# Kernel tuning notes

Hardware: AMD Instinct MI355X
Metric: run time of the kernel (lower is better)

## Reference

```python
import jax, jax.numpy as jnp
import numpy as np

NEG_SLOPE = 0.2
EPS = 1e-9


def setup_inputs() -> dict:
    key = jax.random.key(0)
    ks = jax.random.split(key, 6)
    B, N, E, H, F = 2, 40000, 640000, 4, 32
    X = jax.random.normal(ks[0], (B, N, H, F), dtype=jnp.float32)
    A_self = jax.random.normal(ks[1], (H, F), dtype=jnp.float32)
    A_adjc = jax.random.normal(ks[2], (H, F), dtype=jnp.float32)
    targets = jax.random.randint(ks[3], (B, E), 0, N, dtype=jnp.int32)
    sources = jax.random.randint(ks[4], (B, E), 0, N, dtype=jnp.int32)
    degree = jax.random.uniform(ks[5], (B, E), dtype=jnp.float32)
    return {"X": X, "A_self": A_self, "A_adjc": A_adjc, "degree": degree,
            "targets": targets, "sources": sources, "N": N}


def reference(X, A_self, A_adjc, degree, targets, sources, N):
    # X: [B, N, H, F]; targets/sources: [B, E]
    # per-node attention logits: [B, N, H]
    e_self = jnp.einsum("bnhf,hf->bnh", X, A_self)
    e_adjc = jnp.einsum("bnhf,hf->bnh", X, A_adjc)
    # gather to edges: [B, E, H]
    es = jnp.take_along_axis(e_self, targets[:, :, None], axis=1)
    ea = jnp.take_along_axis(e_adjc, sources[:, :, None], axis=1)
    e = jax.nn.leaky_relu(es + ea, negative_slope=NEG_SLOPE)

    seg_max = jax.vmap(lambda v, i: jax.ops.segment_max(v, i, num_segments=N))
    seg_sum = jax.vmap(lambda v, i: jax.ops.segment_sum(v, i, num_segments=N))

    # exact normalization from source: exp(e - seg_max(e)), then divide by
    # seg_max of the exponentials (+eps), both gathered back to edges.
    m1 = jnp.take_along_axis(seg_max(e, targets), targets[:, :, None], axis=1)
    e = jnp.exp(e - m1)
    m2 = jnp.take_along_axis(seg_max(e, targets), targets[:, :, None], axis=1)
    attn = (e / (m2 + EPS))[..., None]  # [B, E, H, 1]; dropout omitted (eval)

    # message passing: gather source features, weight, scatter-sum to targets
    msg = jnp.take_along_axis(X, sources[:, :, None, None], axis=1) * attn  # [B,E,H,F]
    out = seg_sum(msg, targets)  # [B, N, H, F]
    return out
```

## Files before the change

### kernel.cpp

```cpp
#include <hip/hip_runtime.h>
#include <stdint.h>

#define BB     2
#define NNODE  40000
#define NEDGE  640000
#define NH     4
#define NF     32
#define NHF    128
#define SEGN   (BB * NNODE)
#define GEDGE  (BB * NEDGE)
#define SLOT   48

#define W      512
#define NBK_B  79
#define NBK    (BB * NBK_B)
#define CAP    9216
#define BLK_E  2048
#define NBLKA  (GEDGE / BLK_E)

static constexpr float NEG_SLOPE = 0.2f;
static constexpr float NEG_BIG   = -3.4e38f;

__global__ void prep_k(const float* __restrict__ X,
                       const float* __restrict__ As,
                       const float* __restrict__ Aa,
                       float* __restrict__ S, float* __restrict__ A,
                       unsigned* __restrict__ cursor) {
    int idx = blockIdx.x * blockDim.x + threadIdx.x;
    if (idx < NBK) cursor[idx] = 0u;
    if (idx >= SEGN * NH) return;
    int h = idx & (NH - 1);
    const float4* xv = (const float4*)(X + (size_t)idx * NF);
    const float4* sv = (const float4*)(As + h * NF);
    const float4* av = (const float4*)(Aa + h * NF);
    float s = 0.f, a = 0.f;
#pragma unroll
    for (int i = 0; i < 8; ++i) {
        float4 x = xv[i];
        float4 ws = sv[i];
        float4 wa = av[i];
        s += x.x * ws.x + x.y * ws.y + x.z * ws.z + x.w * ws.w;
        a += x.x * wa.x + x.y * wa.y + x.z * wa.z + x.w * wa.w;
    }
    S[idx] = s;
    A[idx] = a;
}

__global__ __launch_bounds__(256) void binA_k(const int* __restrict__ tg,
                                              const int* __restrict__ sc,
                                              unsigned* __restrict__ cursor,
                                              unsigned* __restrict__ pairs) {
    __shared__ unsigned hist[NBK];
    __shared__ unsigned lofs[NBK];
    __shared__ unsigned gofs[NBK];
    __shared__ unsigned wsum[4];
    __shared__ unsigned staged[BLK_E];
    __shared__ unsigned char sbk[BLK_E];
    int t = threadIdx.x;
    int base = blockIdx.x * BLK_E;
    for (int i = t; i < NBK; i += 256) hist[i] = 0u;
    __syncthreads();

    unsigned pr[8];
    unsigned short pbk[8], plp[8];
#pragma unroll
    for (int k = 0; k < 8; ++k) {
        int e = base + k * 256 + t;
        int tgv = tg[e], scv = sc[e];
        int b = (e >= NEDGE) ? 1 : 0;
        unsigned bk = (unsigned)(b * NBK_B + (tgv >> 9));
        pr[k]  = ((unsigned)(tgv & (W - 1)) << 16) | (unsigned)scv;
        pbk[k] = (unsigned short)bk;
        plp[k] = (unsigned short)atomicAdd(&hist[bk], 1u);
    }
    __syncthreads();
    {
        int lane = t & 63, w = t >> 6;
        unsigned v = (t < NBK) ? hist[t] : 0u;
        unsigned inc = v;
#pragma unroll
        for (int d = 1; d < 64; d <<= 1) {
            unsigned u = __shfl_up(inc, d);
            if (lane >= d) inc += u;
        }
        if (lane == 63) wsum[w] = inc;
        __syncthreads();
        unsigned woff = 0;
#pragma unroll
        for (int i = 0; i < 3; ++i) { if (i < w) woff += wsum[i]; }
        if (t < NBK) {
            lofs[t] = woff + inc - v;
            if (v > 0u)
                gofs[t] = atomicAdd(&cursor[t], v);
        }
    }
    __syncthreads();
#pragma unroll
    for (int k = 0; k < 8; ++k) {
        unsigned j = lofs[pbk[k]] + plp[k];
        staged[j] = pr[k];
        sbk[j] = (unsigned char)pbk[k];
    }
    __syncthreads();
    for (int j = t; j < BLK_E; j += 256) {
        unsigned bk = sbk[j];
        unsigned dst = gofs[bk] + ((unsigned)j - lofs[bk]);
        if (dst < CAP)
            pairs[(size_t)bk * CAP + dst] = staged[j];
    }
}

__global__ __launch_bounds__(1024) void binB_k(const unsigned* __restrict__ cursor,
                                               const unsigned* __restrict__ pairs,
                                               unsigned short* __restrict__ srt,
                                               unsigned* __restrict__ deg) {
    __shared__ unsigned short loc[W * SLOT];
    __shared__ unsigned dloc[W];
    int t = threadIdx.x;
    int gbk = blockIdx.x;
    int b = gbk / NBK_B;
    int bkloc = gbk - b * NBK_B;
    int node0 = b * NNODE + bkloc * W;
    int wEff = min(W, NNODE - bkloc * W);
    for (int i = t; i < W; i += 1024) dloc[i] = 0u;
    __syncthreads();
    int nE = (int)min(cursor[gbk], (unsigned)CAP);
    const unsigned* pb = pairs + (size_t)gbk * CAP;
    for (int j = t; j < nE; j += 1024) {
        unsigned p = pb[j];
        unsigned tl = p >> 16;
        unsigned pos = atomicAdd(&dloc[tl], 1u);
        if (pos < SLOT)
            loc[tl * SLOT + pos] = (unsigned short)(p & 0xFFFFu);
    }
    __syncthreads();
    unsigned* srt32 = (unsigned*)(srt + (size_t)node0 * SLOT);
    const unsigned* loc32 = (const unsigned*)loc;
    int n32 = wEff * SLOT / 2;
    for (int i = t; i < n32; i += 1024) srt32[i] = loc32[i];
    for (int i = t; i < wEff; i += 1024) deg[node0 + i] = dloc[i];
}

__global__ __launch_bounds__(256) void gather_k(
        const float* __restrict__ X, const float* __restrict__ S,
        const float* __restrict__ A, const unsigned* __restrict__ deg,
        const unsigned short* __restrict__ srt, float* __restrict__ OUT) {
    int node = blockIdx.x * 4 + (threadIdx.x >> 6);
    int t = threadIdx.x & 63;
    int hs = t & 3;
    int es = t >> 2;
    int h32 = t >> 5;
    int q = t & 31;
    int haq = q >> 3;
    int dg = min((int)deg[node], SLOT);
    int bbase = (node >= NNODE) ? NNODE : 0;
    size_t beg = (size_t)node * SLOT;

    float sh = S[node * NH + hs];

    float v[3];
    int   sb[3];
#pragma unroll
    for (int c = 0; c < 3; ++c) {
        int e = 16 * c + es;
        int s0 = bbase;
        float vv = NEG_BIG;
        if (e < dg) {
            s0 = bbase + (int)srt[beg + e];
            vv = sh + A[s0 * NH + hs];
            vv = vv > 0.f ? vv : NEG_SLOPE * vv;
        }
        sb[c] = s0;
        v[c]  = vv;
    }
    float m = fmaxf(fmaxf(v[0], v[1]), v[2]);
    m = fmaxf(m, __shfl_xor(m, 4));
    m = fmaxf(m, __shfl_xor(m, 8));
    m = fmaxf(m, __shfl_xor(m, 16));
    m = fmaxf(m, __shfl_xor(m, 32));
    float w[3];
#pragma unroll
    for (int c = 0; c < 3; ++c)
        w[c] = (16 * c + es < dg) ? __expf(v[c] - m) : 0.f;

    float4 acc = make_float4(0.f, 0.f, 0.f, 0.f);
#pragma unroll
    for (int i = 0; i < 24; ++i) {
        if (2 * i < dg) {
            int e2 = 2 * i + h32;
            float we  = __shfl(w[i >> 3],  4 * (e2 & 15) + haq);
            int   sbe = __shfl(sb[i >> 3], 4 * (e2 & 15));
            const float4 x = *(const float4*)(X + (size_t)sbe * NHF + 4 * q);
            acc.x += x.x * we;
            acc.y += x.y * we;
            acc.z += x.z * we;
            acc.w += x.w * we;
        }
    }
    acc.x += __shfl_xor(acc.x, 32);
    acc.y += __shfl_xor(acc.y, 32);
    acc.z += __shfl_xor(acc.z, 32);
    acc.w += __shfl_xor(acc.w, 32);
    if (t < 32) {
        float4* o = (float4*)(OUT + (size_t)node * NHF + 4 * q);
        *o = acc;
    }
}

extern "C" void kernel_launch(void* const* d_in, const int* in_sizes, int n_in,
                              void* d_out, int out_size, void* d_ws, size_t ws_size,
                              hipStream_t stream) {
    const float* X  = (const float*)d_in[0];
    const float* As = (const float*)d_in[1];
    const float* Aa = (const float*)d_in[2];
    const int* tg = (const int*)d_in[4];
    const int* sc = (const int*)d_in[5];
    float* OUT = (float*)d_out;

    char* ws = (char*)d_ws;
    float*          S      = (float*)ws;
    float*          A      = (float*)(ws + 1280000);
    unsigned*       deg    = (unsigned*)(ws + 2560000);
    unsigned*       cursor = (unsigned*)(ws + 2880000);
    unsigned*       pairs  = (unsigned*)(ws + 2880640);
    unsigned short* srt    = (unsigned short*)(ws + 8705152);

    const int nlog = SEGN * NH;
    prep_k<<<(nlog + 255) / 256, 256, 0, stream>>>(X, As, Aa, S, A, cursor);
    binA_k<<<NBLKA, 256, 0, stream>>>(tg, sc, cursor, pairs);
    binB_k<<<NBK, 1024, 0, stream>>>(cursor, pairs, srt, deg);
    gather_k<<<SEGN / 4, 256, 0, stream>>>(X, S, A, deg, srt, OUT);
}
```

Measured before the change: 219.2 us.

## Fuse four pipeline kernels into one cooperative persistent kernel with grid syncs

Merges the prep, two binning passes and the gather into a single persistent cooperative kernel. Stages are separated by grid-wide syncs instead of separate launches. The second binning pass is split into half-buckets of 256 nodes at 256 threads per block, and nontemporal loads and stores are used for the streaming edge and pair buffers. This removes per-launch gaps and tail effects. The costs are grid.sync overhead, lower occupancy limits, and each half-task reading its whole bucket's pairs twice.

```diff
diff --git a/kernel.cpp b/kernel.cpp
--- a/kernel.cpp
+++ b/kernel.cpp
@@ -1,5 +1,8 @@
 #include <hip/hip_runtime.h>
+#include <hip/hip_cooperative_groups.h>
 #include <stdint.h>
+
+namespace cg = cooperative_groups;
 
 #define BB     2
 #define NNODE  40000
@@ -16,16 +19,218 @@
 #define NBK    (BB * NBK_B)
 #define CAP    9216
 #define BLK_E  2048
-#define NBLKA  (GEDGE / BLK_E)
+#define NCHUNK (GEDGE / BLK_E)
+#define MAXG   1536
 
 static constexpr float NEG_SLOPE = 0.2f;
 static constexpr float NEG_BIG   = -3.4e38f;
 
-__global__ void prep_k(const float* __restrict__ X,
-                       const float* __restrict__ As,
-                       const float* __restrict__ Aa,
-                       float* __restrict__ S, float* __restrict__ A,
-                       unsigned* __restrict__ cursor) {
+union SharedU {
+    struct {
+        unsigned hist[NBK], lofs[NBK], gofs[NBK], wsum[4];
+        unsigned staged[BLK_E];
+        unsigned char sbk[BLK_E];
+    } a;
+    struct {
+        unsigned short loc[256 * SLOT];
+        unsigned dloc[256];
+    } b;
+};
+
+__global__ __launch_bounds__(256, 6) void mega_k(
+        const int* __restrict__ tg, const int* __restrict__ sc,
+        const float* __restrict__ X,
+        const float* __restrict__ As, const float* __restrict__ Aa,
+        float* __restrict__ S, float* __restrict__ A,
+        unsigned* __restrict__ cursor, unsigned* __restrict__ pairs,
+        unsigned short* __restrict__ srt, unsigned* __restrict__ deg,
+        float* __restrict__ OUT) {
+    __shared__ SharedU shm;
+    cg::grid_group grid = cg::this_grid();
+    int t = threadIdx.x;
+    int gtid = blockIdx.x * 256 + t;
+    int gsz = gridDim.x * 256;
+
+    for (int idx = gtid; idx < SEGN * NH; idx += gsz) {
+        int h = idx & (NH - 1);
+        const float4* xv = (const float4*)(X + (size_t)idx * NF);
+        const float4* sv = (const float4*)(As + h * NF);
+        const float4* av = (const float4*)(Aa + h * NF);
+        float s = 0.f, a = 0.f;
+#pragma unroll
+        for (int i = 0; i < 8; ++i) {
+            float4 x = xv[i];
+            float4 ws = sv[i];
+            float4 wa = av[i];
+            s += x.x * ws.x + x.y * ws.y + x.z * ws.z + x.w * ws.w;
+            a += x.x * wa.x + x.y * wa.y + x.z * wa.z + x.w * wa.w;
+        }
+        S[idx] = s;
+        A[idx] = a;
+    }
+    for (int i = gtid; i < NBK; i += gsz) cursor[i] = 0u;
+    grid.sync();
+
+    for (int chunk = blockIdx.x; chunk < NCHUNK; chunk += gridDim.x) {
+        int base = chunk * BLK_E;
+        for (int i = t; i < NBK; i += 256) shm.a.hist[i] = 0u;
+        __syncthreads();
+
+        unsigned pr[8];
+        unsigned short pbk[8], plp[8];
+#pragma unroll
+        for (int k = 0; k < 8; ++k) {
+            int e = base + k * 256 + t;
+            int tgv = __builtin_nontemporal_load(tg + e);
+            int scv = __builtin_nontemporal_load(sc + e);
+            int b = (e >= NEDGE) ? 1 : 0;
+            unsigned bk = (unsigned)(b * NBK_B + (tgv >> 9));
+            pr[k]  = ((unsigned)(tgv & (W - 1)) << 16) | (unsigned)scv;
+            pbk[k] = (unsigned short)bk;
+            plp[k] = (unsigned short)atomicAdd(&shm.a.hist[bk], 1u);
+        }
+        __syncthreads();
+        {
+            int lane = t & 63, w = t >> 6;
+            unsigned v = (t < NBK) ? shm.a.hist[t] : 0u;
+            unsigned inc = v;
+#pragma unroll
+            for (int d = 1; d < 64; d <<= 1) {
+                unsigned u = __shfl_up(inc, d);
+                if (lane >= d) inc += u;
+            }
+            if (lane == 63) shm.a.wsum[w] = inc;
+            __syncthreads();
+            unsigned woff = 0;
+#pragma unroll
+            for (int i = 0; i < 3; ++i) { if (i < w) woff += shm.a.wsum[i]; }
+            if (t < NBK) {
+                shm.a.lofs[t] = woff + inc - v;
+                if (v > 0u)
+                    shm.a.gofs[t] = atomicAdd(&cursor[t], v);
+            }
+        }
+        __syncthreads();
+#pragma unroll
+        for (int k = 0; k < 8; ++k) {
+            unsigned j = shm.a.lofs[pbk[k]] + plp[k];
+            shm.a.staged[j] = pr[k];
+            shm.a.sbk[j] = (unsigned char)pbk[k];
+        }
+        __syncthreads();
+        for (int j = t; j < BLK_E; j += 256) {
+            unsigned bk = shm.a.sbk[j];
+            unsigned dst = shm.a.gofs[bk] + ((unsigned)j - shm.a.lofs[bk]);
+            if (dst < CAP)
+                __builtin_nontemporal_store(shm.a.staged[j],
+                                            pairs + (size_t)bk * CAP + dst);
+        }
+        __syncthreads();
+    }
+    grid.sync();
+
+    for (int task = blockIdx.x; task < NBK * 2; task += gridDim.x) {
+        int gbk = task >> 1, half = task & 1;
+        int b = gbk / NBK_B;
+        int bkloc = gbk - b * NBK_B;
+        int nstart = bkloc * W + half * 256;
+        int wEff = min(256, NNODE - nstart);
+        shm.b.dloc[t] = 0u;
+        __syncthreads();
+        int nE = (wEff > 0) ? (int)min(cursor[gbk], (unsigned)CAP) : 0;
+        const unsigned* pb = pairs + (size_t)gbk * CAP;
+        for (int j = t; j < nE; j += 256) {
+            unsigned p = __builtin_nontemporal_load(pb + j);
+            int tl = (int)(p >> 16) - half * 256;
+            if (0 <= tl && tl < 256) {
+                unsigned pos = atomicAdd(&shm.b.dloc[tl], 1u);
+                if (pos < SLOT)
+                    shm.b.loc[tl * SLOT + pos] = (unsigned short)(p & 0xFFFFu);
+            }
+        }
+        __syncthreads();
+        if (wEff > 0) {
+            int node0 = b * NNODE + nstart;
+            unsigned* srt32 = (unsigned*)(srt + (size_t)node0 * SLOT);
+            const unsigned* loc32 = (const unsigned*)shm.b.loc;
+            int n32 = wEff * SLOT / 2;
+            for (int i = t; i < n32; i += 256)
+                __builtin_nontemporal_store(loc32[i], srt32 + i);
+            for (int i = t; i < wEff; i += 256)
+                __builtin_nontemporal_store(shm.b.dloc[i], deg + node0 + i);
+        }
+        __syncthreads();
+    }
+    grid.sync();
+
+    {
+        int lane = t & 63;
+        int wv = t >> 6;
+        int hs = lane & 3;
+        int es = lane >> 2;
+        int h32 = lane >> 5;
+        int q = lane & 31;
+        int haq = q >> 3;
+        for (int node = blockIdx.x * 4 + wv; node < SEGN; node += gridDim.x * 4) {
+            int dg = min((int)deg[node], SLOT);
+            int bbase = (node >= NNODE) ? NNODE : 0;
+            size_t beg = (size_t)node * SLOT;
+            float sH = S[node * NH + hs];
+
+            float v[3];
+            int   sb[3];
+#pragma unroll
+            for (int c = 0; c < 3; ++c) {
+                int e = 16 * c + es;
+                int s0 = bbase;
+                float vv = NEG_BIG;
+                if (e < dg) {
+                    s0 = bbase + (int)srt[beg + e];
+                    vv = sH + A[s0 * NH + hs];
+                    vv = vv > 0.f ? vv : NEG_SLOPE * vv;
+                }
+                sb[c] = s0;
+                v[c]  = vv;
+            }
+            float m = fmaxf(fmaxf(v[0], v[1]), v[2]);
+            m = fmaxf(m, __shfl_xor(m, 4));
+            m = fmaxf(m, __shfl_xor(m, 8));
+            m = fmaxf(m, __shfl_xor(m, 16));
+            m = fmaxf(m, __shfl_xor(m, 32));
+            float w[3];
+#pragma unroll
+            for (int c = 0; c < 3; ++c)
+                w[c] = (16 * c + es < dg) ? __expf(v[c] - m) : 0.f;
+
+            float4 acc = make_float4(0.f, 0.f, 0.f, 0.f);
+#pragma unroll
+            for (int i = 0; i < 24; ++i) {
+                if (2 * i < dg) {
+                    int e2 = 2 * i + h32;
+                    float we  = __shfl(w[i >> 3],  4 * (e2 & 15) + haq);
+                    int   sbe = __shfl(sb[i >> 3], 4 * (e2 & 15));
+                    const float4 x = *(const float4*)(X + (size_t)sbe * NHF + 4 * q);
+                    acc.x += x.x * we;
+                    acc.y += x.y * we;
+                    acc.z += x.z * we;
+                    acc.w += x.w * we;
+                }
+            }
+            acc.x += __shfl_xor(acc.x, 32);
+            acc.y += __shfl_xor(acc.y, 32);
+            acc.z += __shfl_xor(acc.z, 32);
+            acc.w += __shfl_xor(acc.w, 32);
+            if (lane < 32) {
+                float4* o = (float4*)(OUT + (size_t)node * NHF + 4 * q);
+                *o = acc;
+            }
+        }
+    }
+}
+
+__global__ void prep_k(const float* __restrict__ X, const float* __restrict__ As,
+                       const float* __restrict__ Aa, float* __restrict__ S,
+                       float* __restrict__ A, unsigned* __restrict__ cursor) {
     int idx = blockIdx.x * blockDim.x + threadIdx.x;
     if (idx < NBK) cursor[idx] = 0u;
     if (idx >= SEGN * NH) return;
@@ -36,9 +241,7 @@
     float s = 0.f, a = 0.f;
 #pragma unroll
     for (int i = 0; i < 8; ++i) {
-        float4 x = xv[i];
-        float4 ws = sv[i];
-        float4 wa = av[i];
+        float4 x = xv[i], ws = sv[i], wa = av[i];
         s += x.x * ws.x + x.y * ws.y + x.z * ws.z + x.w * ws.w;
         a += x.x * wa.x + x.y * wa.y + x.z * wa.z + x.w * wa.w;
     }
@@ -50,17 +253,13 @@
                                               const int* __restrict__ sc,
                                               unsigned* __restrict__ cursor,
                                               unsigned* __restrict__ pairs) {
-    __shared__ unsigned hist[NBK];
-    __shared__ unsigned lofs[NBK];
-    __shared__ unsigned gofs[NBK];
-    __shared__ unsigned wsum[4];
+    __shared__ unsigned hist[NBK], lofs[NBK], gofs[NBK], wsum[4];
     __shared__ unsigned staged[BLK_E];
     __shared__ unsigned char sbk[BLK_E];
     int t = threadIdx.x;
     int base = blockIdx.x * BLK_E;
     for (int i = t; i < NBK; i += 256) hist[i] = 0u;
     __syncthreads();
-
     unsigned pr[8];
     unsigned short pbk[8], plp[8];
 #pragma unroll
@@ -90,8 +289,7 @@
         for (int i = 0; i < 3; ++i) { if (i < w) woff += wsum[i]; }
         if (t < NBK) {
             lofs[t] = woff + inc - v;
-            if (v > 0u)
-                gofs[t] = atomicAdd(&cursor[t], v);
+            if (v > 0u) gofs[t] = atomicAdd(&cursor[t], v);
         }
     }
     __syncthreads();
@@ -105,8 +303,7 @@
     for (int j = t; j < BLK_E; j += 256) {
         unsigned bk = sbk[j];
         unsigned dst = gofs[bk] + ((unsigned)j - lofs[bk]);
-        if (dst < CAP)
-            pairs[(size_t)bk * CAP + dst] = staged[j];
+        if (dst < CAP) pairs[(size_t)bk * CAP + dst] = staged[j];
     }
 }
 
@@ -130,8 +327,7 @@
         unsigned p = pb[j];
         unsigned tl = p >> 16;
         unsigned pos = atomicAdd(&dloc[tl], 1u);
-        if (pos < SLOT)
-            loc[tl * SLOT + pos] = (unsigned short)(p & 0xFFFFu);
+        if (pos < SLOT) loc[tl * SLOT + pos] = (unsigned short)(p & 0xFFFFu);
     }
     __syncthreads();
     unsigned* srt32 = (unsigned*)(srt + (size_t)node0 * SLOT);
@@ -147,19 +343,12 @@
         const unsigned short* __restrict__ srt, float* __restrict__ OUT) {
     int node = blockIdx.x * 4 + (threadIdx.x >> 6);
     int t = threadIdx.x & 63;
-    int hs = t & 3;
-    int es = t >> 2;
-    int h32 = t >> 5;
-    int q = t & 31;
-    int haq = q >> 3;
+    int hs = t & 3, es = t >> 2, h32 = t >> 5, q = t & 31, haq = q >> 3;
     int dg = min((int)deg[node], SLOT);
     int bbase = (node >= NNODE) ? NNODE : 0;
     size_t beg = (size_t)node * SLOT;
-
-    float sh = S[node * NH + hs];
-
-    float v[3];
-    int   sb[3];
+    float sH = S[node * NH + hs];
+    float v[3]; int sb[3];
 #pragma unroll
     for (int c = 0; c < 3; ++c) {
         int e = 16 * c + es;
@@ -167,11 +356,10 @@
         float vv = NEG_BIG;
         if (e < dg) {
             s0 = bbase + (int)srt[beg + e];
-            vv = sh + A[s0 * NH + hs];
+            vv = sH + A[s0 * NH + hs];
             vv = vv > 0.f ? vv : NEG_SLOPE * vv;
         }
-        sb[c] = s0;
-        v[c]  = vv;
+        sb[c] = s0; v[c] = vv;
     }
     float m = fmaxf(fmaxf(v[0], v[1]), v[2]);
     m = fmaxf(m, __shfl_xor(m, 4));
@@ -182,7 +370,6 @@
 #pragma unroll
     for (int c = 0; c < 3; ++c)
         w[c] = (16 * c + es < dg) ? __expf(v[c] - m) : 0.f;
-
     float4 acc = make_float4(0.f, 0.f, 0.f, 0.f);
 #pragma unroll
     for (int i = 0; i < 24; ++i) {
@@ -191,20 +378,15 @@
             float we  = __shfl(w[i >> 3],  4 * (e2 & 15) + haq);
             int   sbe = __shfl(sb[i >> 3], 4 * (e2 & 15));
             const float4 x = *(const float4*)(X + (size_t)sbe * NHF + 4 * q);
-            acc.x += x.x * we;
-            acc.y += x.y * we;
-            acc.z += x.z * we;
-            acc.w += x.w * we;
+            acc.x += x.x * we; acc.y += x.y * we;
+            acc.z += x.z * we; acc.w += x.w * we;
         }
     }
     acc.x += __shfl_xor(acc.x, 32);
     acc.y += __shfl_xor(acc.y, 32);
     acc.z += __shfl_xor(acc.z, 32);
     acc.w += __shfl_xor(acc.w, 32);
-    if (t < 32) {
-        float4* o = (float4*)(OUT + (size_t)node * NHF + 4 * q);
-        *o = acc;
-    }
+    if (t < 32) *(float4*)(OUT + (size_t)node * NHF + 4 * q) = acc;
 }
 
 extern "C" void kernel_launch(void* const* d_in, const int* in_sizes, int n_in,
@@ -225,9 +407,34 @@
     unsigned*       pairs  = (unsigned*)(ws + 2880640);
     unsigned short* srt    = (unsigned short*)(ws + 8705152);
 
-    const int nlog = SEGN * NH;
-    prep_k<<<(nlog + 255) / 256, 256, 0, stream>>>(X, As, Aa, S, A, cursor);
-    binA_k<<<NBLKA, 256, 0, stream>>>(tg, sc, cursor, pairs);
-    binB_k<<<NBK, 1024, 0, stream>>>(cursor, pairs, srt, deg);
-    gather_k<<<SEGN / 4, 256, 0, stream>>>(X, S, A, deg, srt, OUT);
-}
+    static int G = 0;
+    if (G == 0) {
+        int nb = 0;
+        hipError_t oc = hipOccupancyMaxActiveBlocksPerMultiprocessor(&nb, mega_k, 256, 0);
+        int cus = 0;
+        hipDeviceGetAttribute(&cus, hipDeviceAttributeMultiprocessorCount, 0);
+        if (oc != hipSuccess || nb <= 0 || cus <= 0) G = -1;
+        else {
+            G = nb * cus;
+            if (G > MAXG) G = MAXG;
+        }
+    }
+
+    bool launched = false;
+    if (G > 0) {
+        void* args[] = {(void*)&tg, (void*)&sc, (void*)&X, (void*)&As, (void*)&Aa,
+                        (void*)&S, (void*)&A, (void*)&cursor, (void*)&pairs,
+                        (void*)&srt, (void*)&deg, (void*)&OUT};
+        hipError_t rc = hipLaunchCooperativeKernel((void*)mega_k, dim3(G), dim3(256),
+                                                   args, 0, stream);
+        if (rc == hipSuccess) launched = true;
+        else G = -1;
+    }
+    if (!launched) {
+        const int nlog = SEGN * NH;
+        prep_k<<<(nlog + 255) / 256, 256, 0, stream>>>(X, As, Aa, S, A, cursor);
+        binA_k<<<NCHUNK, 256, 0, stream>>>(tg, sc, cursor, pairs);
+        binB_k<<<NBK, 1024, 0, stream>>>(cursor, pairs, srt, deg);
+        gather_k<<<SEGN / 4, 256, 0, stream>>>(X, S, A, deg, srt, OUT);
+    }
+}
```

After: 563.6 us. +157.1%, slower.

## Replace two-pass binning with direct fine-bucket scatter and fuse sort into gather

Applied to the files above, without the earlier changes.

The block-level histogram/prefix-scan binning kernel is replaced by direct global atomics into 64-node fine buckets, split into 4 replica cursors to reduce atomic contention. The second binning pass is fused into the gather kernel, which builds per-node adjacency lists in shared memory and then processes 16 nodes per wavefront. This removes one kernel launch and the srt/deg round trip through global memory. In exchange it relies on global atomics and on fixed per-replica capacity (384), which could overflow for skewed inputs. Cursor reset moves to hipMemsetAsync and the loads and stores use nontemporal hints.

```diff
diff --git a/kernel.cpp b/kernel.cpp
--- a/kernel.cpp
+++ b/kernel.cpp
@@ -11,24 +11,24 @@
 #define GEDGE  (BB * NEDGE)
 #define SLOT   48
 
-#define W      512
-#define NBK_B  79
-#define NBK    (BB * NBK_B)
-#define CAP    9216
+#define FW     64
+#define NFB_B  625
+#define NFB    (BB * NFB_B)
+#define NREP   4
+#define RCAP   384
+#define CAPF   (NREP * RCAP)
 #define BLK_E  2048
-#define NBLKA  (GEDGE / BLK_E)
+#define NBLKD  (GEDGE / BLK_E)
 
 static constexpr float NEG_SLOPE = 0.2f;
 static constexpr float NEG_BIG   = -3.4e38f;
 
-__global__ void prep_k(const float* __restrict__ X,
-                       const float* __restrict__ As,
-                       const float* __restrict__ Aa,
-                       float* __restrict__ S, float* __restrict__ A,
-                       unsigned* __restrict__ cursor) {
+__global__ __launch_bounds__(256) void prep_k(const float* __restrict__ X,
+                                              const float* __restrict__ As,
+                                              const float* __restrict__ Aa,
+                                              float* __restrict__ S,
+                                              float* __restrict__ A) {
     int idx = blockIdx.x * blockDim.x + threadIdx.x;
-    if (idx < NBK) cursor[idx] = 0u;
-    if (idx >= SEGN * NH) return;
     int h = idx & (NH - 1);
     const float4* xv = (const float4*)(X + (size_t)idx * NF);
     const float4* sv = (const float4*)(As + h * NF);
@@ -46,164 +46,118 @@
     A[idx] = a;
 }
 
-__global__ __launch_bounds__(256) void binA_k(const int* __restrict__ tg,
+__global__ __launch_bounds__(256) void binD_k(const int* __restrict__ tg,
                                               const int* __restrict__ sc,
-                                              unsigned* __restrict__ cursor,
+                                              unsigned* __restrict__ cursor4,
                                               unsigned* __restrict__ pairs) {
-    __shared__ unsigned hist[NBK];
-    __shared__ unsigned lofs[NBK];
-    __shared__ unsigned gofs[NBK];
-    __shared__ unsigned wsum[4];
-    __shared__ unsigned staged[BLK_E];
-    __shared__ unsigned char sbk[BLK_E];
     int t = threadIdx.x;
     int base = blockIdx.x * BLK_E;
-    for (int i = t; i < NBK; i += 256) hist[i] = 0u;
-    __syncthreads();
-
-    unsigned pr[8];
-    unsigned short pbk[8], plp[8];
+    int rep = blockIdx.x & (NREP - 1);
 #pragma unroll
     for (int k = 0; k < 8; ++k) {
         int e = base + k * 256 + t;
-        int tgv = tg[e], scv = sc[e];
+        int tgv = __builtin_nontemporal_load(tg + e);
+        int scv = __builtin_nontemporal_load(sc + e);
         int b = (e >= NEDGE) ? 1 : 0;
-        unsigned bk = (unsigned)(b * NBK_B + (tgv >> 9));
-        pr[k]  = ((unsigned)(tgv & (W - 1)) << 16) | (unsigned)scv;
-        pbk[k] = (unsigned short)bk;
-        plp[k] = (unsigned short)atomicAdd(&hist[bk], 1u);
+        int fb = b * NFB_B + (tgv >> 6);
+        unsigned pos = atomicAdd(&cursor4[fb * NREP + rep], 1u);
+        if (pos < RCAP)
+            __builtin_nontemporal_store(
+                ((unsigned)(tgv & (FW - 1)) << 16) | (unsigned)scv,
+                pairs + (size_t)fb * CAPF + rep * RCAP + pos);
     }
+}
+
+__global__ __launch_bounds__(256) void gat_k(const float* __restrict__ X,
+                                             const float* __restrict__ S,
+                                             const float* __restrict__ A,
+                                             const unsigned* __restrict__ cursor4,
+                                             const unsigned* __restrict__ pairs,
+                                             float* __restrict__ OUT) {
+    __shared__ unsigned short loc[FW * SLOT];
+    __shared__ unsigned dloc[FW];
+    int t = threadIdx.x;
+    int fb = blockIdx.x;
+    int b = fb / NFB_B;
+    int node0 = b * NNODE + (fb - b * NFB_B) * FW;
+    int bbase = b * NNODE;
+    if (t < FW) dloc[t] = 0u;
     __syncthreads();
-    {
-        int lane = t & 63, w = t >> 6;
-        unsigned v = (t < NBK) ? hist[t] : 0u;
-        unsigned inc = v;
 #pragma unroll
-        for (int d = 1; d < 64; d <<= 1) {
-            unsigned u = __shfl_up(inc, d);
-            if (lane >= d) inc += u;
-        }
-        if (lane == 63) wsum[w] = inc;
-        __syncthreads();
-        unsigned woff = 0;
-#pragma unroll
-        for (int i = 0; i < 3; ++i) { if (i < w) woff += wsum[i]; }
-        if (t < NBK) {
-            lofs[t] = woff + inc - v;
-            if (v > 0u)
-                gofs[t] = atomicAdd(&cursor[t], v);
+    for (int r = 0; r < NREP; ++r) {
+        int c = (int)min(cursor4[fb * NREP + r], (unsigned)RCAP);
+        const unsigned* pb = pairs + (size_t)fb * CAPF + r * RCAP;
+        for (int j = t; j < c; j += 256) {
+            unsigned p = __builtin_nontemporal_load(pb + j);
+            unsigned tl = p >> 16;
+            unsigned pos = atomicAdd(&dloc[tl], 1u);
+            if (pos < SLOT)
+                loc[tl * SLOT + pos] = (unsigned short)(p & 0xFFFFu);
         }
     }
     __syncthreads();
+
+    int lane = t & 63;
+    int hs = lane & 3;
+    int es = lane >> 2;
+    int h32 = lane >> 5;
+    int q = lane & 31;
+    int haq = q >> 3;
+    int nlbase = (t >> 6) * 16;
+    for (int it = 0; it < 16; ++it) {
+        int nl = nlbase + it;
+        int node = node0 + nl;
+        int dg = min((int)dloc[nl], SLOT);
+        const unsigned short* sl = loc + nl * SLOT;
+        float sH = S[node * NH + hs];
+
+        float v[3];
+        int   sb[3];
 #pragma unroll
-    for (int k = 0; k < 8; ++k) {
-        unsigned j = lofs[pbk[k]] + plp[k];
-        staged[j] = pr[k];
-        sbk[j] = (unsigned char)pbk[k];
-    }
-    __syncthreads();
-    for (int j = t; j < BLK_E; j += 256) {
-        unsigned bk = sbk[j];
-        unsigned dst = gofs[bk] + ((unsigned)j - lofs[bk]);
-        if (dst < CAP)
-            pairs[(size_t)bk * CAP + dst] = staged[j];
-    }
-}
+        for (int c = 0; c < 3; ++c) {
+            int e = 16 * c + es;
+            int s0 = bbase;
+            float vv = NEG_BIG;
+            if (e < dg) {
+                s0 = bbase + (int)sl[e];
+                vv = sH + A[s0 * NH + hs];
+                vv = vv > 0.f ? vv : NEG_SLOPE * vv;
+            }
+            sb[c] = s0;
+            v[c]  = vv;
+        }
+        float m = fmaxf(fmaxf(v[0], v[1]), v[2]);
+        m = fmaxf(m, __shfl_xor(m, 4));
+        m = fmaxf(m, __shfl_xor(m, 8));
+        m = fmaxf(m, __shfl_xor(m, 16));
+        m = fmaxf(m, __shfl_xor(m, 32));
+        float w[3];
+#pragma unroll
+        for (int c = 0; c < 3; ++c)
+            w[c] = (16 * c + es < dg) ? __expf(v[c] - m) : 0.f;
 
-__global__ __launch_bounds__(1024) void binB_k(const unsigned* __restrict__ cursor,
-                                               const unsigned* __restrict__ pairs,
-                                               unsigned short* __restrict__ srt,
-                                               unsigned* __restrict__ deg) {
-    __shared__ unsigned short loc[W * SLOT];
-    __shared__ unsigned dloc[W];
-    int t = threadIdx.x;
-    int gbk = blockIdx.x;
-    int b = gbk / NBK_B;
-    int bkloc = gbk - b * NBK_B;
-    int node0 = b * NNODE + bkloc * W;
-    int wEff = min(W, NNODE - bkloc * W);
-    for (int i = t; i < W; i += 1024) dloc[i] = 0u;
-    __syncthreads();
-    int nE = (int)min(cursor[gbk], (unsigned)CAP);
-    const unsigned* pb = pairs + (size_t)gbk * CAP;
-    for (int j = t; j < nE; j += 1024) {
-        unsigned p = pb[j];
-        unsigned tl = p >> 16;
-        unsigned pos = atomicAdd(&dloc[tl], 1u);
-        if (pos < SLOT)
-            loc[tl * SLOT + pos] = (unsigned short)(p & 0xFFFFu);
-    }
-    __syncthreads();
-    unsigned* srt32 = (unsigned*)(srt + (size_t)node0 * SLOT);
-    const unsigned* loc32 = (const unsigned*)loc;
-    int n32 = wEff * SLOT / 2;
-    for (int i = t; i < n32; i += 1024) srt32[i] = loc32[i];
-    for (int i = t; i < wEff; i += 1024) deg[node0 + i] = dloc[i];
-}
-
-__global__ __launch_bounds__(256) void gather_k(
-        const float* __restrict__ X, const float* __restrict__ S,
-        const float* __restrict__ A, const unsigned* __restrict__ deg,
-        const unsigned short* __restrict__ srt, float* __restrict__ OUT) {
-    int node = blockIdx.x * 4 + (threadIdx.x >> 6);
-    int t = threadIdx.x & 63;
-    int hs = t & 3;
-    int es = t >> 2;
-    int h32 = t >> 5;
-    int q = t & 31;
-    int haq = q >> 3;
-    int dg = min((int)deg[node], SLOT);
-    int bbase = (node >= NNODE) ? NNODE : 0;
-    size_t beg = (size_t)node * SLOT;
-
-    float sh = S[node * NH + hs];
-
-    float v[3];
-    int   sb[3];
+        float4 acc = make_float4(0.f, 0.f, 0.f, 0.f);
 #pragma unroll
-    for (int c = 0; c < 3; ++c) {
-        int e = 16 * c + es;
-        int s0 = bbase;
-        float vv = NEG_BIG;
-        if (e < dg) {
-            s0 = bbase + (int)srt[beg + e];
-            vv = sh + A[s0 * NH + hs];
-            vv = vv > 0.f ? vv : NEG_SLOPE * vv;
+        for (int i = 0; i < 24; ++i) {
+            if (2 * i < dg) {
+                int e2 = 2 * i + h32;
+                float we  = __shfl(w[i >> 3],  4 * (e2 & 15) + haq);
+                int   sbe = __shfl(sb[i >> 3], 4 * (e2 & 15));
+                const float4 x = *(const float4*)(X + (size_t)sbe * NHF + 4 * q);
+                acc.x += x.x * we;
+                acc.y += x.y * we;
+                acc.z += x.z * we;
+                acc.w += x.w * we;
+            }
         }
-        sb[c] = s0;
-        v[c]  = vv;
-    }
-    float m = fmaxf(fmaxf(v[0], v[1]), v[2]);
-    m = fmaxf(m, __shfl_xor(m, 4));
-    m = fmaxf(m, __shfl_xor(m, 8));
-    m = fmaxf(m, __shfl_xor(m, 16));
-    m = fmaxf(m, __shfl_xor(m, 32));
-    float w[3];
-#pragma unroll
-    for (int c = 0; c < 3; ++c)
-        w[c] = (16 * c + es < dg) ? __expf(v[c] - m) : 0.f;
-
-    float4 acc = make_float4(0.f, 0.f, 0.f, 0.f);
-#pragma unroll
-    for (int i = 0; i < 24; ++i) {
-        if (2 * i < dg) {
-            int e2 = 2 * i + h32;
-            float we  = __shfl(w[i >> 3],  4 * (e2 & 15) + haq);
-            int   sbe = __shfl(sb[i >> 3], 4 * (e2 & 15));
-            const float4 x = *(const float4*)(X + (size_t)sbe * NHF + 4 * q);
-            acc.x += x.x * we;
-            acc.y += x.y * we;
-            acc.z += x.z * we;
-            acc.w += x.w * we;
+        acc.x += __shfl_xor(acc.x, 32);
+        acc.y += __shfl_xor(acc.y, 32);
+        acc.z += __shfl_xor(acc.z, 32);
+        acc.w += __shfl_xor(acc.w, 32);
+        if (lane < 32) {
+            float4* o = (float4*)(OUT + (size_t)node * NHF + 4 * q);
+            *o = acc;
         }
-    }
-    acc.x += __shfl_xor(acc.x, 32);
-    acc.y += __shfl_xor(acc.y, 32);
-    acc.z += __shfl_xor(acc.z, 32);
-    acc.w += __shfl_xor(acc.w, 32);
-    if (t < 32) {
-        float4* o = (float4*)(OUT + (size_t)node * NHF + 4 * q);
-        *o = acc;
     }
 }
 
@@ -218,16 +172,13 @@
     float* OUT = (float*)d_out;
 
     char* ws = (char*)d_ws;
-    float*          S      = (float*)ws;
-    float*          A      = (float*)(ws + 1280000);
-    unsigned*       deg    = (unsigned*)(ws + 2560000);
-    unsigned*       cursor = (unsigned*)(ws + 2880000);
-    unsigned*       pairs  = (unsigned*)(ws + 2880640);
-    unsigned short* srt    = (unsigned short*)(ws + 8705152);
+    float*    S       = (float*)ws;
+    float*    A       = (float*)(ws + 1280000);
+    unsigned* cursor4 = (unsigned*)(ws + 2560000);
+    unsigned* pairs   = (unsigned*)(ws + 2580000);
 
-    const int nlog = SEGN * NH;
-    prep_k<<<(nlog + 255) / 256, 256, 0, stream>>>(X, As, Aa, S, A, cursor);
-    binA_k<<<NBLKA, 256, 0, stream>>>(tg, sc, cursor, pairs);
-    binB_k<<<NBK, 1024, 0, stream>>>(cursor, pairs, srt, deg);
-    gather_k<<<SEGN / 4, 256, 0, stream>>>(X, S, A, deg, srt, OUT);
+    hipMemsetAsync(cursor4, 0, NFB * NREP * sizeof(unsigned), stream);
+    prep_k<<<SEGN * NH / 256, 256, 0, stream>>>(X, As, Aa, S, A);
+    binD_k<<<NBLKD, 256, 0, stream>>>(tg, sc, cursor4, pairs);
+    gat_k<<<NFB, 256, 0, stream>>>(X, S, A, cursor4, pairs, OUT);
 }
```

New measurement: 305.6 us. 39.4% more time.

## Split gather per head and half-feature with XCD-aware block mapping

Applied to the files above, without the earlier changes.

The gather kernel now gives each wavefront one (node, head, 16-feature half) slice and launches 8x more blocks. Block IDs are mapped so each XCD handles one (head, batch) pair, which keeps the matching X slices local to that XCD's L2. The per-node logits are stored head-major to suit this. Each wave reads only 64B per source row and recomputes the softmax weights for its slice, which adds redundant srt, deg and logit reads and more cross-lane reductions. It also adds non-temporal loads and stores.

```diff
diff --git a/kernel.cpp b/kernel.cpp
--- a/kernel.cpp
+++ b/kernel.cpp
@@ -21,15 +21,18 @@
 static constexpr float NEG_SLOPE = 0.2f;
 static constexpr float NEG_BIG   = -3.4e38f;
 
+typedef float vf4 __attribute__((ext_vector_type(4)));
+
 __global__ void prep_k(const float* __restrict__ X,
                        const float* __restrict__ As,
                        const float* __restrict__ Aa,
-                       float* __restrict__ S, float* __restrict__ A,
+                       float* __restrict__ S2, float* __restrict__ A2,
                        unsigned* __restrict__ cursor) {
     int idx = blockIdx.x * blockDim.x + threadIdx.x;
     if (idx < NBK) cursor[idx] = 0u;
     if (idx >= SEGN * NH) return;
     int h = idx & (NH - 1);
+    int gnode = idx >> 2;
     const float4* xv = (const float4*)(X + (size_t)idx * NF);
     const float4* sv = (const float4*)(As + h * NF);
     const float4* av = (const float4*)(Aa + h * NF);
@@ -42,8 +45,8 @@
         s += x.x * ws.x + x.y * ws.y + x.z * ws.z + x.w * ws.w;
         a += x.x * wa.x + x.y * wa.y + x.z * wa.z + x.w * wa.w;
     }
-    S[idx] = s;
-    A[idx] = a;
+    S2[(size_t)h * SEGN + gnode] = s;
+    A2[(size_t)h * SEGN + gnode] = a;
 }
 
 __global__ __launch_bounds__(256) void binA_k(const int* __restrict__ tg,
@@ -141,69 +144,67 @@
     for (int i = t; i < wEff; i += 1024) deg[node0 + i] = dloc[i];
 }
 
-__global__ __launch_bounds__(256) void gather_k(
-        const float* __restrict__ X, const float* __restrict__ S,
-        const float* __restrict__ A, const unsigned* __restrict__ deg,
+__global__ __launch_bounds__(256) void gath_k(
+        const float* __restrict__ X, const float* __restrict__ S2,
+        const float* __restrict__ A2, const unsigned* __restrict__ deg,
         const unsigned short* __restrict__ srt, float* __restrict__ OUT) {
-    int node = blockIdx.x * 4 + (threadIdx.x >> 6);
-    int t = threadIdx.x & 63;
-    int hs = t & 3;
-    int es = t >> 2;
-    int h32 = t >> 5;
-    int q = t & 31;
-    int haq = q >> 3;
-    int dg = min((int)deg[node], SLOT);
-    int bbase = (node >= NNODE) ? NNODE : 0;
+    int bid = blockIdx.x;
+    int xcd = bid & 7;
+    int h   = xcd >> 1;
+    int bb  = xcd & 1;
+    int rest = bid >> 3;
+    int half = (rest >= 10000) ? 1 : 0;
+    int sub  = rest - half * 10000;
+    int lane = threadIdx.x & 63;
+    int node = bb * NNODE + sub * 4 + (threadIdx.x >> 6);
+
+    int dg = min((int)__builtin_nontemporal_load(deg + node), SLOT);
     size_t beg = (size_t)node * SLOT;
-
-    float sh = S[node * NH + hs];
-
-    float v[3];
-    int   sb[3];
-#pragma unroll
-    for (int c = 0; c < 3; ++c) {
-        int e = 16 * c + es;
-        int s0 = bbase;
-        float vv = NEG_BIG;
-        if (e < dg) {
-            s0 = bbase + (int)srt[beg + e];
-            vv = sh + A[s0 * NH + hs];
-            vv = vv > 0.f ? vv : NEG_SLOPE * vv;
-        }
-        sb[c] = s0;
-        v[c]  = vv;
-    }
-    float m = fmaxf(fmaxf(v[0], v[1]), v[2]);
+    float sH = S2[(size_t)h * SEGN + node];
+
+    unsigned s16 = 0u;
+    if (lane < 48) s16 = __builtin_nontemporal_load(srt + beg + lane);
+    int sbv = bb * NNODE + (int)min(s16, NNODE - 1u);
+    int sb0 = __shfl(sbv, 0);
+    int sb  = (lane < dg) ? sbv : sb0;
+    float vv = NEG_BIG;
+    if (lane < dg) {
+        vv = sH + A2[(size_t)h * SEGN + sb];
+        vv = vv > 0.f ? vv : NEG_SLOPE * vv;
+    }
+    float m = vv;
+    m = fmaxf(m, __shfl_xor(m, 1));
+    m = fmaxf(m, __shfl_xor(m, 2));
     m = fmaxf(m, __shfl_xor(m, 4));
     m = fmaxf(m, __shfl_xor(m, 8));
     m = fmaxf(m, __shfl_xor(m, 16));
     m = fmaxf(m, __shfl_xor(m, 32));
-    float w[3];
-#pragma unroll
-    for (int c = 0; c < 3; ++c)
-        w[c] = (16 * c + es < dg) ? __expf(v[c] - m) : 0.f;
-
-    float4 acc = make_float4(0.f, 0.f, 0.f, 0.f);
-#pragma unroll
-    for (int i = 0; i < 24; ++i) {
-        if (2 * i < dg) {
-            int e2 = 2 * i + h32;
-            float we  = __shfl(w[i >> 3],  4 * (e2 & 15) + haq);
-            int   sbe = __shfl(sb[i >> 3], 4 * (e2 & 15));
-            const float4 x = *(const float4*)(X + (size_t)sbe * NHF + 4 * q);
-            acc.x += x.x * we;
-            acc.y += x.y * we;
-            acc.z += x.z * we;
-            acc.w += x.w * we;
+    float w = (lane < dg) ? __expf(vv - m) : 0.f;
+
+    int c  = lane >> 2;
+    int qq = lane & 3;
+    vf4 acc = (vf4)(0.f);
+#pragma unroll
+    for (int i = 0; i < 3; ++i) {
+        if (16 * i < dg) {
+            int e = 16 * i + c;
+            float we  = __shfl(w, e);
+            int   sbe = __shfl(sb, e);
+            const vf4 x = *(const vf4*)(X + (size_t)sbe * NHF + h * NF + half * 16 + 4 * qq);
+            acc += x * we;
         }
     }
-    acc.x += __shfl_xor(acc.x, 32);
-    acc.y += __shfl_xor(acc.y, 32);
-    acc.z += __shfl_xor(acc.z, 32);
-    acc.w += __shfl_xor(acc.w, 32);
-    if (t < 32) {
-        float4* o = (float4*)(OUT + (size_t)node * NHF + 4 * q);
-        *o = acc;
+    acc.x += __shfl_xor(acc.x, 4);  acc.y += __shfl_xor(acc.y, 4);
+    acc.z += __shfl_xor(acc.z, 4);  acc.w += __shfl_xor(acc.w, 4);
+    acc.x += __shfl_xor(acc.x, 8);  acc.y += __shfl_xor(acc.y, 8);
+    acc.z += __shfl_xor(acc.z, 8);  acc.w += __shfl_xor(acc.w, 8);
+    acc.x += __shfl_xor(acc.x, 16); acc.y += __shfl_xor(acc.y, 16);
+    acc.z += __shfl_xor(acc.z, 16); acc.w += __shfl_xor(acc.w, 16);
+    acc.x += __shfl_xor(acc.x, 32); acc.y += __shfl_xor(acc.y, 32);
+    acc.z += __shfl_xor(acc.z, 32); acc.w += __shfl_xor(acc.w, 32);
+    if (c == 0) {
+        __builtin_nontemporal_store(acc,
+            (vf4*)(OUT + (size_t)node * NHF + h * NF + half * 16 + 4 * qq));
     }
 }
 
@@ -218,16 +219,16 @@
     float* OUT = (float*)d_out;
 
     char* ws = (char*)d_ws;
-    float*          S      = (float*)ws;
-    float*          A      = (float*)(ws + 1280000);
+    float*          S2     = (float*)ws;
+    float*          A2     = (float*)(ws + 1280000);
     unsigned*       deg    = (unsigned*)(ws + 2560000);
     unsigned*       cursor = (unsigned*)(ws + 2880000);
     unsigned*       pairs  = (unsigned*)(ws + 2880640);
     unsigned short* srt    = (unsigned short*)(ws + 8705152);
 
     const int nlog = SEGN * NH;
-    prep_k<<<(nlog + 255) / 256, 256, 0, stream>>>(X, As, Aa, S, A, cursor);
+    prep_k<<<(nlog + 255) / 256, 256, 0, stream>>>(X, As, Aa, S2, A2, cursor);
     binA_k<<<NBLKA, 256, 0, stream>>>(tg, sc, cursor, pairs);
     binB_k<<<NBK, 1024, 0, stream>>>(cursor, pairs, srt, deg);
-    gather_k<<<SEGN / 4, 256, 0, stream>>>(X, S, A, deg, srt, OUT);
-}
+    gath_k<<<160000, 256, 0, stream>>>(X, S2, A2, deg, srt, OUT);
+}
```

Measured after the change: 346.3 us. 58.0% more time.
